# Optimization experiments

Measured on AMD Instinct MI355X. Metric: run time of the kernel, lower is better.

The kernel has to match this reference:

```python
import jax, jax.numpy as jnp
import numpy as np

TEMPERATURE = 0.5
TAU_PLUS = 0.1
EPS = 1e-8


def setup_inputs() -> dict:
    key = jax.random.key(0)
    k1, k2 = jax.random.split(key)
    B, D = 8192, 128
    z_i = jax.random.normal(k1, (B, D), dtype=jnp.float32)
    z_j = jax.random.normal(k2, (B, D), dtype=jnp.float32)
    return {"z_i": z_i, "z_j": z_j}


def _l2_normalize(x, axis=1, eps=1e-12):
    # matches torch F.normalize: x / max(||x||, eps)
    n = jnp.linalg.norm(x, axis=axis, keepdims=True)
    return x / jnp.maximum(n, eps)


def reference(z_i, z_j):
    B = z_i.shape[0]
    zi = _l2_normalize(z_i, axis=1)
    zj = _l2_normalize(z_j, axis=1)
    reps = jnp.concatenate([zi, zj], axis=0)  # [2B, D]
    sim = jnp.matmul(reps, reps.T) / TEMPERATURE  # [2B, 2B]
    sim = sim - jnp.max(sim, axis=1, keepdims=True)
    mask = jnp.eye(2 * B, dtype=bool)
    sim = jnp.where(mask, -9e15, sim)
    pos = jnp.exp(jnp.sum(zi * zj, axis=-1) / TEMPERATURE)  # [B]
    positives = jnp.concatenate([pos, pos], axis=0)  # [2B]
    neg_sum = jnp.sum(jnp.exp(sim), axis=1)  # [2B]
    Ng = (-TAU_PLUS * B * positives + neg_sum) / (1.0 - TAU_PLUS)
    Ng = jnp.maximum(Ng, B * jnp.exp(jnp.asarray(-1.0 / TEMPERATURE, dtype=sim.dtype)))
    loss = -jnp.log(positives / (positives + Ng + EPS))
    return jnp.mean(loss)
```

## Files before the change

### kernel.cpp

```cpp
#include <hip/hip_runtime.h>
#include <hip/hip_bf16.h>

typedef __attribute__((ext_vector_type(8))) short bf16x8;
typedef __attribute__((ext_vector_type(4))) float f32x4;

#define B_ROWS 8192
#define NROWS 16384
#define D 128
#define C1 2.8853900817779268f
#define E_M2 0.13533528323661270f
#define RSCALE 1.6986436f
#define JSPLIT 16
#define COLS (NROWS / JSPLIT)
#define TILE_COLS 64
#define TILE_BYTES (TILE_COLS * D * 2)
#define NT (COLS / TILE_COLS)

__device__ __forceinline__ float fast_exp2(float x) {
#if __has_builtin(__builtin_amdgcn_exp2f)
    return __builtin_amdgcn_exp2f(x);
#else
    float r; asm("v_exp_f32 %0, %1" : "=v"(r) : "v"(x)); return r;
#endif
}
__device__ __forceinline__ float fast_log2(float x) {
#if __has_builtin(__builtin_amdgcn_logf)
    return __builtin_amdgcn_logf(x);
#else
    float r; asm("v_log_f32 %0, %1" : "=v"(r) : "v"(x)); return r;
#endif
}

__device__ __forceinline__ unsigned short f2bf(float f) {
    union { float f; unsigned u; } v; v.f = f;
    unsigned r = v.u + 0x7FFFu + ((v.u >> 16) & 1u);
    return (unsigned short)(r >> 16);
}

__global__ __launch_bounds__(256) void k_norm(const float* __restrict__ zi,
                                              const float* __restrict__ zj,
                                              unsigned* __restrict__ repsU,
                                              float* __restrict__ pos) {
    int w = threadIdx.x >> 6, lane = threadIdx.x & 63;
    int row = blockIdx.x * 4 + w;
    const float2* a2 = (const float2*)(zi + (size_t)row * D);
    const float2* b2 = (const float2*)(zj + (size_t)row * D);
    float2 a = a2[lane], b = b2[lane];
    float si = a.x * a.x + a.y * a.y;
    float sj = b.x * b.x + b.y * b.y;
    float sd = a.x * b.x + a.y * b.y;
#pragma unroll
    for (int m = 32; m; m >>= 1) {
        si += __shfl_xor(si, m);
        sj += __shfl_xor(sj, m);
        sd += __shfl_xor(sd, m);
    }
    float inv_i = 1.0f / fmaxf(sqrtf(si), 1e-12f);
    float inv_j = 1.0f / fmaxf(sqrtf(sj), 1e-12f);
    float sa = inv_i * RSCALE, sb = inv_j * RSCALE;
    repsU[(size_t)row * 64 + lane] =
        (unsigned)f2bf(a.x * sa) | ((unsigned)f2bf(a.y * sa) << 16);
    repsU[(size_t)(row + B_ROWS) * 64 + lane] =
        (unsigned)f2bf(b.x * sb) | ((unsigned)f2bf(b.y * sb) << 16);
    if (lane == 0) pos[row] = fast_exp2(sd * inv_i * inv_j * C1);
}

__global__ __launch_bounds__(256, 2) void k_negsum(const unsigned short* __restrict__ R,
                                                   float* __restrict__ partial) {
    __shared__ char smem[2][TILE_BYTES];
    int js = blockIdx.x & (JSPLIT - 1);
    int rowBase = (blockIdx.x >> 4) * 256;
    int w = threadIdx.x >> 6;
    int lane = threadIdx.x & 63;
    int lr = lane & 15, lk = lane >> 4;
    int waveRow = rowBase + w * 64;

    bf16x8 afrag[4][4];
#pragma unroll
    for (int r = 0; r < 4; ++r)
#pragma unroll
        for (int kk = 0; kk < 4; ++kk)
            afrag[r][kk] = *(const bf16x8*)(R + (size_t)(waveRow + r * 16 + lr) * D + kk * 32 + lk * 8);

    int srcoff[4], dstoff[4];
#pragma unroll
    for (int j = 0; j < 4; ++j) {
        int o = (w * 4 + j) * 1024 + lane * 16;
        int row = o >> 8, c = o & 255;
        srcoff[j] = row * 256 + (c ^ ((row & 7) << 4));
        dstoff[j] = (w * 4 + j) * 1024;
    }

    int colStart = js * COLS;
    const char* Rb = (const char*)R;
    int tdiag = (waveRow - colStart) >> 6;

    int m64 = (lr & 4) << 4;
    int lbase = lr * 256 + ((lk * 16) ^ ((lr & 3) << 4));

    float acc[4][4] = {};

#define STAGE(buf, t)                                                             \
    do {                                                                          \
        const char* tb_ = Rb + (size_t)(colStart + (t) * TILE_COLS) * 256;        \
        _Pragma("unroll")                                                         \
        for (int j = 0; j < 4; ++j)                                               \
            __builtin_amdgcn_global_load_lds(                                     \
                (const __attribute__((address_space(1))) unsigned*)(tb_ + srcoff[j]), \
                (__attribute__((address_space(3))) unsigned*)(&smem[buf][dstoff[j]]), \
                16, 0, 0);                                                        \
    } while (0)

#define BATCH_BODY(DIAG)                                                          \
    do {                                                                          \
        _Pragma("unroll")                                                         \
        for (int ct = 0; ct < 4; ++ct) {                                          \
            _Pragma("unroll")                                                     \
            for (int r = 0; r < 4; ++r) {                                         \
                f32x4 c = {0.f, 0.f, 0.f, 0.f};                                   \
                c = __builtin_amdgcn_mfma_f32_16x16x32_bf16(afrag[r][0], bf[ct][0], c, 0, 0, 0); \
                c = __builtin_amdgcn_mfma_f32_16x16x32_bf16(afrag[r][1], bf[ct][1], c, 0, 0, 0); \
                c = __builtin_amdgcn_mfma_f32_16x16x32_bf16(afrag[r][2], bf[ct][2], c, 0, 0, 0); \
                c = __builtin_amdgcn_mfma_f32_16x16x32_bf16(afrag[r][3], bf[ct][3], c, 0, 0, 0); \
                if (DIAG && ct == r) {                                            \
                    _Pragma("unroll")                                             \
                    for (int q = 0; q < 4; ++q)                                   \
                        if (lk * 4 + q != lr) acc[r][q] += fast_exp2(c[q]);       \
                } else {                                                          \
                    _Pragma("unroll")                                             \
                    for (int q = 0; q < 4; ++q) acc[r][q] += fast_exp2(c[q]);     \
                }                                                                 \
            }                                                                     \
        }                                                                         \
    } while (0)

    STAGE(0, 0);
    __syncthreads();
    int cur = 0;
    for (int t = 0; t < NT; ++t) {
        if (t + 1 < NT) STAGE(cur ^ 1, t + 1);
        const char* sb = &smem[cur][0] + lbase;
        bf16x8 bf[4][4];
#pragma unroll
        for (int ct = 0; ct < 4; ++ct)
#pragma unroll
            for (int kk = 0; kk < 4; ++kk)
                bf[ct][kk] = *(const bf16x8*)(sb + ct * 4096 + ((kk * 64) ^ m64));
        if (t == tdiag) {
            BATCH_BODY(true);
        } else {
            BATCH_BODY(false);
        }
        __syncthreads();
        cur ^= 1;
    }
#undef STAGE
#undef BATCH_BODY

#pragma unroll
    for (int r = 0; r < 4; ++r)
#pragma unroll
        for (int q = 0; q < 4; ++q) {
            float v = acc[r][q];
            v += __shfl_xor(v, 1);
            v += __shfl_xor(v, 2);
            v += __shfl_xor(v, 4);
            v += __shfl_xor(v, 8);
            if (lr == 0)
                partial[(size_t)js * NROWS + waveRow + r * 16 + lk * 4 + q] = v;
        }
}

__global__ __launch_bounds__(256) void k_loss1(const float* __restrict__ pos,
                                               const float* __restrict__ partial,
                                               float* __restrict__ bsum) {
    int i = blockIdx.x * 256 + threadIdx.x;
    float neg = 0.f;
#pragma unroll
    for (int s = 0; s < JSPLIT; ++s) neg += partial[(size_t)s * NROWS + i];
    neg *= E_M2;
    float p = pos[i & (B_ROWS - 1)];
    float Ng = fmaxf((neg - 819.2f * p) * (1.0f / 0.9f), 8192.0f * E_M2);
    float l = fast_log2((p + Ng + 1e-8f) / p) * 0.69314718056f;
#pragma unroll
    for (int m = 32; m; m >>= 1) l += __shfl_xor(l, m);
    __shared__ float s4[4];
    int wv = threadIdx.x >> 6;
    if ((threadIdx.x & 63) == 0) s4[wv] = l;
    __syncthreads();
    if (threadIdx.x == 0) bsum[blockIdx.x] = s4[0] + s4[1] + s4[2] + s4[3];
}

__global__ void k_loss2(const float* __restrict__ bsum, float* __restrict__ out) {
    float v = bsum[threadIdx.x];
#pragma unroll
    for (int m = 32; m; m >>= 1) v += __shfl_xor(v, m);
    if (threadIdx.x == 0) out[0] = v * (1.0f / (float)NROWS);
}

extern "C" void kernel_launch(void* const* d_in, const int* in_sizes, int n_in,
                              void* d_out, int out_size, void* d_ws, size_t ws_size,
                              hipStream_t stream) {
    const float* zi = (const float*)d_in[0];
    const float* zj = (const float*)d_in[1];
    unsigned short* reps = (unsigned short*)d_ws;
    float* pos = (float*)((char*)d_ws + (size_t)NROWS * D * 2);
    float* partial = pos + B_ROWS;
    float* bsum = partial + (size_t)JSPLIT * NROWS;
    float* out = (float*)d_out;

    k_norm<<<B_ROWS / 4, 256, 0, stream>>>(zi, zj, (unsigned*)reps, pos);
    k_negsum<<<64 * JSPLIT, 256, 0, stream>>>(reps, partial);
    k_loss1<<<NROWS / 256, 256, 0, stream>>>(pos, partial, bsum);
    k_loss2<<<1, 64, 0, stream>>>(bsum, out);
}
```

Baseline: 79.47 us.

## Exploit symmetry of similarity matrix to compute only upper-triangular tiles

```diff
diff --git a/kernel.cpp b/kernel.cpp
--- a/kernel.cpp
+++ b/kernel.cpp
@@ -10,11 +10,10 @@
 #define C1 2.8853900817779268f
 #define E_M2 0.13533528323661270f
 #define RSCALE 1.6986436f
-#define JSPLIT 16
-#define COLS (NROWS / JSPLIT)
+#define NSPLIT 16
+#define NCHUNK 64
 #define TILE_COLS 64
 #define TILE_BYTES (TILE_COLS * D * 2)
-#define NT (COLS / TILE_COLS)
 
 __device__ __forceinline__ float fast_exp2(float x) {
 #if __has_builtin(__builtin_amdgcn_exp2f)
@@ -66,10 +65,13 @@
 }
 
 __global__ __launch_bounds__(256, 2) void k_negsum(const unsigned short* __restrict__ R,
-                                                   float* __restrict__ partial) {
+                                                   float* __restrict__ rowpart,
+                                                   float* __restrict__ colpart) {
     __shared__ char smem[2][TILE_BYTES];
-    int js = blockIdx.x & (JSPLIT - 1);
-    int rowBase = (blockIdx.x >> 4) * 256;
+    __shared__ float colredL[2][4][64];
+    int I = blockIdx.x >> 4;
+    int s = blockIdx.x & (NSPLIT - 1);
+    int rowBase = I << 8;
     int w = threadIdx.x >> 6;
     int lane = threadIdx.x & 63;
     int lr = lane & 15, lk = lane >> 4;
@@ -91,18 +93,20 @@
         dstoff[j] = (w * 4 + j) * 1024;
     }
 
-    int colStart = js * COLS;
+    int dph = (s - ((I << 2) & 15)) & 15;
+    int jstart = (I << 2) + dph;
+    int nt = (jstart < 256) ? (((255 - jstart) >> 4) + 1) : 0;
+
     const char* Rb = (const char*)R;
-    int tdiag = (waveRow - colStart) >> 6;
 
     int m64 = (lr & 4) << 4;
     int lbase = lr * 256 + ((lk * 16) ^ ((lr & 3) << 4));
 
     float acc[4][4] = {};
 
-#define STAGE(buf, t)                                                             \
+#define STAGE(buf, jj)                                                            \
     do {                                                                          \
-        const char* tb_ = Rb + (size_t)(colStart + (t) * TILE_COLS) * 256;        \
+        const char* tb_ = Rb + (size_t)(jj) * (TILE_COLS * 256);                  \
         _Pragma("unroll")                                                         \
         for (int j = 0; j < 4; ++j)                                               \
             __builtin_amdgcn_global_load_lds(                                     \
@@ -125,20 +129,34 @@
                 if (DIAG && ct == r) {                                            \
                     _Pragma("unroll")                                             \
                     for (int q = 0; q < 4; ++q)                                   \
-                        if (lk * 4 + q != lr) acc[r][q] += fast_exp2(c[q]);       \
+                        if (lk * 4 + q != lr) {                                   \
+                            float e = fast_exp2(c[q]);                            \
+                            acc[r][q] += e; csum[ct] += e;                        \
+                        }                                                         \
                 } else {                                                          \
                     _Pragma("unroll")                                             \
-                    for (int q = 0; q < 4; ++q) acc[r][q] += fast_exp2(c[q]);     \
+                    for (int q = 0; q < 4; ++q) {                                 \
+                        float e = fast_exp2(c[q]);                                \
+                        acc[r][q] += e; csum[ct] += e;                            \
+                    }                                                             \
                 }                                                                 \
             }                                                                     \
         }                                                                         \
     } while (0)
 
-    STAGE(0, 0);
+    if (nt > 0) STAGE(0, jstart);
     __syncthreads();
     int cur = 0;
-    for (int t = 0; t < NT; ++t) {
-        if (t + 1 < NT) STAGE(cur ^ 1, t + 1);
+    int prevColBase = -1, prevBuf = 0;
+    for (int t = 0; t < nt; ++t) {
+        int jt = jstart + (t << 4);
+        int colBase = jt << 6;
+        if (prevColBase >= 0 && w == ((t + 3) & 3)) {
+            float v = colredL[prevBuf][0][lane] + colredL[prevBuf][1][lane] +
+                      colredL[prevBuf][2][lane] + colredL[prevBuf][3][lane];
+            colpart[(size_t)I * NROWS + prevColBase + lane] = v;
+        }
+        if (t + 1 < nt) STAGE(cur ^ 1, jt + 16);
         const char* sb = &smem[cur][0] + lbase;
         bf16x8 bf[4][4];
 #pragma unroll
@@ -146,13 +164,31 @@
 #pragma unroll
             for (int kk = 0; kk < 4; ++kk)
                 bf[ct][kk] = *(const bf16x8*)(sb + ct * 4096 + ((kk * 64) ^ m64));
-        if (t == tdiag) {
+        float csum[4] = {0.f, 0.f, 0.f, 0.f};
+        bool offdiag = (colBase >= rowBase + 256);
+        if (colBase == waveRow) {
             BATCH_BODY(true);
         } else {
             BATCH_BODY(false);
         }
+        if (offdiag) {
+#pragma unroll
+            for (int ct = 0; ct < 4; ++ct) {
+                float v = csum[ct];
+                v += __shfl_xor(v, 16);
+                v += __shfl_xor(v, 32);
+                if (lk == 0) colredL[cur][w][ct * 16 + lr] = v;
+            }
+        }
         __syncthreads();
+        prevColBase = offdiag ? colBase : -1;
+        prevBuf = cur;
         cur ^= 1;
+    }
+    if (prevColBase >= 0 && w == ((nt + 3) & 3)) {
+        float v = colredL[prevBuf][0][lane] + colredL[prevBuf][1][lane] +
+                  colredL[prevBuf][2][lane] + colredL[prevBuf][3][lane];
+        colpart[(size_t)I * NROWS + prevColBase + lane] = v;
     }
 #undef STAGE
 #undef BATCH_BODY
@@ -167,17 +203,20 @@
             v += __shfl_xor(v, 4);
             v += __shfl_xor(v, 8);
             if (lr == 0)
-                partial[(size_t)js * NROWS + waveRow + r * 16 + lk * 4 + q] = v;
+                rowpart[(size_t)s * NROWS + waveRow + r * 16 + lk * 4 + q] = v;
         }
 }
 
 __global__ __launch_bounds__(256) void k_loss1(const float* __restrict__ pos,
-                                               const float* __restrict__ partial,
+                                               const float* __restrict__ rowpart,
+                                               const float* __restrict__ colpart,
                                                float* __restrict__ bsum) {
     int i = blockIdx.x * 256 + threadIdx.x;
     float neg = 0.f;
 #pragma unroll
-    for (int s = 0; s < JSPLIT; ++s) neg += partial[(size_t)s * NROWS + i];
+    for (int s = 0; s < NSPLIT; ++s) neg += rowpart[(size_t)s * NROWS + i];
+    int M = i >> 8;
+    for (int I = 0; I < M; ++I) neg += colpart[(size_t)I * NROWS + i];
     neg *= E_M2;
     float p = pos[i & (B_ROWS - 1)];
     float Ng = fmaxf((neg - 819.2f * p) * (1.0f / 0.9f), 8192.0f * E_M2);
@@ -205,12 +244,13 @@
     const float* zj = (const float*)d_in[1];
     unsigned short* reps = (unsigned short*)d_ws;
     float* pos = (float*)((char*)d_ws + (size_t)NROWS * D * 2);
-    float* partial = pos + B_ROWS;
-    float* bsum = partial + (size_t)JSPLIT * NROWS;
+    float* rowpart = pos + B_ROWS;
+    float* colpart = rowpart + (size_t)NSPLIT * NROWS;
+    float* bsum = colpart + (size_t)NCHUNK * NROWS;
     float* out = (float*)d_out;
 
     k_norm<<<B_ROWS / 4, 256, 0, stream>>>(zi, zj, (unsigned*)reps, pos);
-    k_negsum<<<64 * JSPLIT, 256, 0, stream>>>(reps, partial);
-    k_loss1<<<NROWS / 256, 256, 0, stream>>>(pos, partial, bsum);
+    k_negsum<<<NCHUNK * NSPLIT, 256, 0, stream>>>(reps, rowpart, colpart);
+    k_loss1<<<NROWS / 256, 256, 0, stream>>>(pos, rowpart, colpart, bsum);
     k_loss2<<<1, 64, 0, stream>>>(bsum, out);
 }
```

New measurement: 82.56 us. +3.9%, slower.
